# Kernel tuning notes

Measured on AMD Instinct MI355X. Metric: run time of the kernel, lower is better.

Reference implementation:

```python
import jax, jax.numpy as jnp
import numpy as np

_LN_EPS = 1e-5

def _gelu(x):
    return jax.nn.gelu(x, approximate=False)

def _layernorm(x, g, b):
    mu = x.mean(-1, keepdims=True)
    var = ((x - mu) ** 2).mean(-1, keepdims=True)
    return (x - mu) * jax.lax.rsqrt(var + _LN_EPS) * g + b

def setup_inputs() -> dict:
    key = jax.random.key(0)
    ks = jax.random.split(key, 8)
    B, S, D = 4, 2048, 1024
    N_IN, N_PROC, D_R = 8192, 4096, 256
    s = 0.02
    return {
        "x": jax.random.normal(ks[0], (B, S, D), jnp.float32),
        "W1": jax.random.normal(ks[1], (2 * D_R, D), jnp.float32) * s,
        "b1": jnp.zeros((2 * D_R,), jnp.float32),
        "ln_g": jnp.ones((2 * D_R,), jnp.float32),
        "ln_b": jnp.zeros((2 * D_R,), jnp.float32),
        "W2": jax.random.normal(ks[2], (D_R, 2 * D_R), jnp.float32) * s,
        "b2": jnp.zeros((D_R,), jnp.float32),
        "neuron_keys": jax.random.normal(ks[3], (N_IN, D_R), jnp.float32) * s,
        "input_patterns": jax.random.normal(ks[4], (N_IN, D), jnp.float32) * s,
        "process_weights": jax.random.normal(ks[5], (N_PROC, N_IN), jnp.float32) * s,
        "process_outputs": jax.random.normal(ks[6], (N_PROC, D), jnp.float32) * s,
        "k_input": 4096,
        "k_process": 2048,
    }

def reference(x, W1, b1, ln_g, ln_b, W2, b2, neuron_keys, input_patterns,
              process_weights, process_outputs, k_input, k_process):
    d_routing = neuron_keys.shape[1]
    # --- Global router: sequence max-pool context -> query -> top-k input neurons
    gc = x.max(axis=1)                                   # [B, D]
    h = _layernorm(_gelu(gc @ W1.T + b1), ln_g, ln_b)    # [B, 2*d_r]
    query = h @ W2.T + b2                                # [B, d_r]
    logits = (query @ neuron_keys.T) / jnp.sqrt(jnp.asarray(d_routing, x.dtype))  # [B, N_in]
    _, input_idx = jax.lax.top_k(logits, k_input)        # [B, k_in]
    # --- Input neuron activations, gather selected ones
    input_acts = _gelu(jnp.einsum('bsd,nd->bsn', x, input_patterns))   # [B,S,N_in]
    sel_acts = jnp.take_along_axis(input_acts, input_idx[:, None, :], axis=2)  # [B,S,k_in]
    # --- Per-batch gather of process weight columns, process activations
    W_sel = jnp.take(process_weights, input_idx, axis=1)               # [N_proc,B,k_in]
    proc_acts = _gelu(jnp.einsum('bsk,pbk->bsp', sel_acts, W_sel))     # [B,S,N_proc]
    scores = proc_acts.mean(axis=1)                                    # [B,N_proc]
    _, proc_idx = jax.lax.top_k(scores, k_process)                     # [B,k_proc]
    sel_proc = jnp.take_along_axis(proc_acts, proc_idx[:, None, :], axis=2)  # [B,S,k_proc]
    out_w = process_outputs[proc_idx]                                  # [B,k_proc,D]
    return jnp.einsum('bsk,bkd->bsd', sel_proc, out_w)                 # [B,S,D]
```

## Files before the change

### kernel.cpp

```cpp
#include <hip/hip_runtime.h>
#include <cstdint>

#define B_    4
#define S_    2048
#define D_    1024
#define NIN   8192
#define NPROC 4096
#define DR    256
#define DR2   512
#define KIN   4096
#define KPROC 2048

typedef _Float16 v8h __attribute__((ext_vector_type(8)));
typedef _Float16 v4h __attribute__((ext_vector_type(4)));
typedef float    v4f __attribute__((ext_vector_type(4)));

__device__ __forceinline__ float geluf(float v) {
    return 0.5f * v * (1.0f + erff(v * 0.70710678f));
}

__device__ __forceinline__ void cp16(void* lds, const void* g) {
    __builtin_amdgcn_global_load_lds(
        (const __attribute__((address_space(1))) unsigned int*)g,
        (__attribute__((address_space(3))) unsigned int*)lds, 16, 0, 0);
}

__global__ void k_conv_x16(const float* __restrict__ x, _Float16* __restrict__ x16, int n4) {
    int i = blockIdx.x * 256 + threadIdx.x;
    if (i < n4) {
        float4 v = ((const float4*)x)[i];
        v4h h = { (_Float16)v.x, (_Float16)v.y, (_Float16)v.z, (_Float16)v.w };
        ((v4h*)x16)[i] = h;
    }
}

__global__ void k_conv_split(const float* __restrict__ p, _Float16* __restrict__ ph,
                             _Float16* __restrict__ pl, int n) {
    int i = blockIdx.x * 256 + threadIdx.x;
    if (i < n) {
        float v = p[i];
        _Float16 h = (_Float16)v;
        ph[i] = h;
        pl[i] = (_Float16)(v - (float)h);
    }
}

__global__ void k_max1(const float* __restrict__ x, float* __restrict__ pmax) {
    int d = blockIdx.x * 256 + threadIdx.x;
    int chunk = blockIdx.y;
    int b = blockIdx.z;
    const float* base = x + ((size_t)b * S_ + chunk * 128) * D_ + d;
    float m = -3.4e38f;
    for (int s = 0; s < 128; s++) m = fmaxf(m, base[(size_t)s * D_]);
    pmax[((size_t)b * 16 + chunk) * D_ + d] = m;
}

__global__ void k_max2(const float* __restrict__ pmax, double* __restrict__ gc64) {
    int d = blockIdx.x * 256 + threadIdx.x;
    int b = blockIdx.y;
    float m = -3.4e38f;
    for (int c = 0; c < 16; c++) m = fmaxf(m, pmax[((size_t)b * 16 + c) * D_ + d]);
    gc64[(size_t)b * D_ + d] = (double)m;
}

__global__ __launch_bounds__(256) void k_router1(
    const double* __restrict__ gc64, const float* __restrict__ W1, const float* __restrict__ b1,
    double* __restrict__ hpre)
{
    int wave = threadIdx.x >> 6, lane = threadIdx.x & 63;
    int j = blockIdx.x * 4 + wave;
    int b = blockIdx.y;
    const double* g = gc64 + (size_t)b * D_;
    const float* w = W1 + (size_t)j * D_;
    double acc = 0.0;
    for (int d = lane; d < D_; d += 64) acc += g[d] * (double)w[d];
#pragma unroll
    for (int o = 32; o > 0; o >>= 1) acc += __shfl_xor(acc, o, 64);
    if (lane == 0) {
        double z = acc + (double)b1[j];
        hpre[(size_t)b * DR2 + j] = 0.5 * z * (1.0 + erf(z * 0.7071067811865475244));
    }
}

__global__ __launch_bounds__(512) void k_router2(
    const double* __restrict__ hpre, const float* __restrict__ lng, const float* __restrict__ lnb,
    const float* __restrict__ W2, const float* __restrict__ b2, double* __restrict__ qs)
{
    __shared__ double sh[DR2];
    __shared__ double red[DR2];
    int b = blockIdx.x, j = threadIdx.x;
    double ge = hpre[(size_t)b * DR2 + j];
    sh[j] = ge; red[j] = ge;
    __syncthreads();
    for (int s = 256; s > 0; s >>= 1) { if (j < s) red[j] += red[j + s]; __syncthreads(); }
    double mu = red[0] / 512.0;
    __syncthreads();
    double dv = ge - mu;
    red[j] = dv * dv;
    __syncthreads();
    for (int s = 256; s > 0; s >>= 1) { if (j < s) red[j] += red[j + s]; __syncthreads(); }
    double rs = 1.0 / sqrt(red[0] / 512.0 + 1e-5);
    __syncthreads();
    sh[j] = dv * rs * (double)lng[j] + (double)lnb[j];
    __syncthreads();
    if (j < DR) {
        double q = (double)b2[j];
        const float* w2r = W2 + (size_t)j * DR2;
        for (int t = 0; t < DR2; t++) q += sh[t] * (double)w2r[t];
        qs[(size_t)b * DR + j] = q;
    }
}

__global__ __launch_bounds__(256) void k_router3(
    const double* __restrict__ qs, const float* __restrict__ keys, double* __restrict__ logits)
{
    int wave = threadIdx.x >> 6, lane = threadIdx.x & 63;
    int n = blockIdx.x * 4 + wave;
    int b = blockIdx.y;
    const double* q = qs + (size_t)b * DR;
    const float* kr = keys + (size_t)n * DR;
    double acc = 0.0;
#pragma unroll
    for (int t = 0; t < 4; t++) {
        int d = lane + t * 64;
        acc += q[d] * (double)kr[d];
    }
#pragma unroll
    for (int o = 32; o > 0; o >>= 1) acc += __shfl_xor(acc, o, 64);
    if (lane == 0) logits[(size_t)b * NIN + n] = acc * 0.0625;
}

template<int N, int K>
__global__ __launch_bounds__(1024) void k_topk(const double* __restrict__ vals, int* __restrict__ outIdx) {
    __shared__ unsigned long long keys[N];
    int b = blockIdx.x, tid = threadIdx.x;
    for (int i = tid; i < N; i += 1024) {
        float v = (float)vals[(size_t)b * N + i];
        unsigned int u = __float_as_uint(v);
        u = (u & 0x80000000u) ? ~u : (u | 0x80000000u);
        keys[i] = ((unsigned long long)u << 32) | (unsigned int)(~i);
    }
    __syncthreads();
    for (int k = 2; k <= N; k <<= 1)
        for (int j = k >> 1; j > 0; j >>= 1) {
            for (int i = tid; i < N; i += 1024) {
                int l = i ^ j;
                if (l > i) {
                    unsigned long long a = keys[i], c = keys[l];
                    bool up = ((i & k) == 0);
                    if ((a < c) == up) { keys[i] = c; keys[l] = a; }
                }
            }
            __syncthreads();
        }
    for (int i = tid; i < K; i += 1024)
        outIdx[(size_t)b * K + i] = (int)(~(unsigned int)keys[i]);
}

__global__ void k_gatherW(const float* __restrict__ pw, const int* __restrict__ iidx,
                          _Float16* __restrict__ Wh, _Float16* __restrict__ Wl,
                          int b_base, size_t wstride) {
    int p = blockIdx.x;
    int b = b_base + blockIdx.y;
    const float* row = pw + (size_t)p * NIN;
    const int* ix = iidx + (size_t)b * KIN;
    _Float16* wh = Wh + (size_t)blockIdx.y * wstride + (size_t)p * KIN;
    _Float16* wl = Wl + (size_t)blockIdx.y * wstride + (size_t)p * KIN;
    for (int j = threadIdx.x; j < KIN; j += 256) {
        float w = row[ix[j]];
        _Float16 h = (_Float16)w;
        wh[j] = h;
        wl[j] = (_Float16)(w - (float)h);
    }
}

__global__ void k_gatherSP(const _Float16* __restrict__ acts16, const int* __restrict__ pidx,
                           _Float16* __restrict__ sp) {
    int s = blockIdx.x, b = blockIdx.y;
    const _Float16* arow = acts16 + ((size_t)b * S_ + s) * NPROC;
    _Float16* orow = sp + ((size_t)b * S_ + s) * KPROC;
    const int* pi = pidx + (size_t)b * KPROC;
    for (int k = threadIdx.x; k < KPROC; k += 256) orow[k] = arow[pi[k]];
}

__global__ void k_gatherWoT(const _Float16* __restrict__ pout16, const int* __restrict__ pidx,
                            _Float16* __restrict__ woT) {
    __shared__ _Float16 t[64][65];
    int k0 = blockIdx.x * 64, d0 = blockIdx.y * 64, b = blockIdx.z;
    const int* pi = pidx + (size_t)b * KPROC;
    for (int i = threadIdx.x; i < 4096; i += 256) {
        int kk = i >> 6, dd = i & 63;
        t[kk][dd] = pout16[(size_t)pi[k0 + kk] * D_ + d0 + dd];
    }
    __syncthreads();
    for (int i = threadIdx.x; i < 4096; i += 256) {
        int dd = i >> 6, kk = i & 63;
        woT[((size_t)b * D_ + d0 + dd) * KPROC + k0 + kk] = t[kk][dd];
    }
}


__global__ __launch_bounds__(256, 3) void k_gemmD(
    const _Float16* __restrict__ x16, const _Float16* __restrict__ ph, const _Float16* __restrict__ pl,
    const int* __restrict__ iidx, _Float16* __restrict__ a16)
{
    const int b = blockIdx.z;
    const int m0 = blockIdx.x * 128, n0 = blockIdx.y * 128;
    __shared__ _Float16 tA[4096], tBh[4096], tBl[4096];
    const int tid = threadIdx.x, lane = tid & 63;
    const int wave = tid >> 6, wrow = wave >> 1, wcol = wave & 1;
    const int srow = tid >> 2, spart = tid & 3;
    const int spe = spart ^ ((srow >> 1) & 3);

    const _Float16* as0 = x16 + ((size_t)b * S_ + m0 + srow) * D_ + spe * 8;
    const _Float16* as1 = as0 + (size_t)64 * D_;
    int r0 = iidx[(size_t)b * KIN + n0 + srow];
    int r1 = iidx[(size_t)b * KIN + n0 + srow + 64];
    const _Float16* bh0 = ph + (size_t)r0 * D_ + spe * 8;
    const _Float16* bh1 = ph + (size_t)r1 * D_ + spe * 8;
    const _Float16* bl0 = pl + (size_t)r0 * D_ + spe * 8;
    const _Float16* bl1 = pl + (size_t)r1 * D_ + spe * 8;

    v4f acc[4][4];
    v4f z = {0.f, 0.f, 0.f, 0.f};
#pragma unroll
    for (int i = 0; i < 4; i++)
#pragma unroll
        for (int j = 0; j < 4; j++) acc[i][j] = z;

    const int swz = ((lane & 15) >> 1) & 3;
    const int aoff = (wrow * 64 + (lane & 15)) * 32 + ((lane >> 4) ^ swz) * 8;
    const int boff = (wcol * 64 + (lane & 15)) * 32 + ((lane >> 4) ^ swz) * 8;

    for (int kt = 0; kt < D_; kt += 32) {
        __syncthreads();
        cp16(&tA[tid * 8], as0 + kt);
        cp16(&tA[2048 + tid * 8], as1 + kt);
        cp16(&tBh[tid * 8], bh0 + kt);
        cp16(&tBh[2048 + tid * 8], bh1 + kt);
        cp16(&tBl[tid * 8], bl0 + kt);
        cp16(&tBl[2048 + tid * 8], bl1 + kt);
        asm volatile("s_waitcnt vmcnt(0)" ::: "memory");
        __syncthreads();
        v8h af[4], fh[4], fl[4];
#pragma unroll
        for (int i = 0; i < 4; i++) af[i] = *(const v8h*)&tA[aoff + i * 512];
#pragma unroll
        for (int j = 0; j < 4; j++) {
            fh[j] = *(const v8h*)&tBh[boff + j * 512];
            fl[j] = *(const v8h*)&tBl[boff + j * 512];
        }
#pragma unroll
        for (int i = 0; i < 4; i++)
#pragma unroll
            for (int j = 0; j < 4; j++) {
                acc[i][j] = __builtin_amdgcn_mfma_f32_16x16x32_f16(af[i], fh[j], acc[i][j], 0, 0, 0);
                acc[i][j] = __builtin_amdgcn_mfma_f32_16x16x32_f16(af[i], fl[j], acc[i][j], 0, 0, 0);
            }
    }
    const int rbase = m0 + wrow * 64 + ((lane >> 4) << 2);
    const int cbase = n0 + wcol * 64 + (lane & 15);
#pragma unroll
    for (int i = 0; i < 4; i++)
#pragma unroll
        for (int j = 0; j < 4; j++)
#pragma unroll
            for (int r = 0; r < 4; r++) {
                float gv = geluf(acc[i][j][r]);
                a16[((size_t)b * S_ + rbase + i * 16 + r) * (size_t)KIN + cbase + j * 16] = (_Float16)gv;
            }
}

__global__ __launch_bounds__(256, 3) void k_gemmE(
    const _Float16* __restrict__ a16, const _Float16* __restrict__ Wh, const _Float16* __restrict__ Wl,
    _Float16* __restrict__ acts16, double* __restrict__ scores, int b_base, size_t wstride)
{
    const int b = b_base + blockIdx.z;
    const int m0 = blockIdx.x * 128, n0 = blockIdx.y * 128;
    __shared__ _Float16 tA[4096], tBh[4096], tBl[4096];
    const int tid = threadIdx.x, lane = tid & 63;
    const int wave = tid >> 6, wrow = wave >> 1, wcol = wave & 1;
    const int srow = tid >> 2, spart = tid & 3;
    const int spe = spart ^ ((srow >> 1) & 3);

    const _Float16* as0 = a16 + ((size_t)b * S_ + m0 + srow) * (size_t)KIN + spe * 8;
    const _Float16* as1 = as0 + (size_t)64 * KIN;
    const _Float16* whB = Wh + (size_t)blockIdx.z * wstride;
    const _Float16* wlB = Wl + (size_t)blockIdx.z * wstride;
    const _Float16* bh0 = whB + (size_t)(n0 + srow) * KIN + spe * 8;
    const _Float16* bh1 = bh0 + (size_t)64 * KIN;
    const _Float16* bl0 = wlB + (size_t)(n0 + srow) * KIN + spe * 8;
    const _Float16* bl1 = bl0 + (size_t)64 * KIN;

    v4f acc[4][4];
    v4f z = {0.f, 0.f, 0.f, 0.f};
#pragma unroll
    for (int i = 0; i < 4; i++)
#pragma unroll
        for (int j = 0; j < 4; j++) acc[i][j] = z;

    const int swz = ((lane & 15) >> 1) & 3;
    const int aoff = (wrow * 64 + (lane & 15)) * 32 + ((lane >> 4) ^ swz) * 8;
    const int boff = (wcol * 64 + (lane & 15)) * 32 + ((lane >> 4) ^ swz) * 8;

    for (int kt = 0; kt < KIN; kt += 32) {
        __syncthreads();
        cp16(&tA[tid * 8], as0 + kt);
        cp16(&tA[2048 + tid * 8], as1 + kt);
        cp16(&tBh[tid * 8], bh0 + kt);
        cp16(&tBh[2048 + tid * 8], bh1 + kt);
        cp16(&tBl[tid * 8], bl0 + kt);
        cp16(&tBl[2048 + tid * 8], bl1 + kt);
        asm volatile("s_waitcnt vmcnt(0)" ::: "memory");
        __syncthreads();
        v8h af[4], fh[4], fl[4];
#pragma unroll
        for (int i = 0; i < 4; i++) af[i] = *(const v8h*)&tA[aoff + i * 512];
#pragma unroll
        for (int j = 0; j < 4; j++) {
            fh[j] = *(const v8h*)&tBh[boff + j * 512];
            fl[j] = *(const v8h*)&tBl[boff + j * 512];
        }
#pragma unroll
        for (int i = 0; i < 4; i++)
#pragma unroll
            for (int j = 0; j < 4; j++) {
                acc[i][j] = __builtin_amdgcn_mfma_f32_16x16x32_f16(af[i], fh[j], acc[i][j], 0, 0, 0);
                acc[i][j] = __builtin_amdgcn_mfma_f32_16x16x32_f16(af[i], fl[j], acc[i][j], 0, 0, 0);
            }
    }
    const int rbase = m0 + wrow * 64 + ((lane >> 4) << 2);
    const int cbase = n0 + wcol * 64 + (lane & 15);
    float psum[4] = {0.f, 0.f, 0.f, 0.f};
#pragma unroll
    for (int i = 0; i < 4; i++)
#pragma unroll
        for (int j = 0; j < 4; j++)
#pragma unroll
            for (int r = 0; r < 4; r++) {
                float gv = geluf(acc[i][j][r]);
                acts16[((size_t)b * S_ + rbase + i * 16 + r) * (size_t)NPROC + cbase + j * 16] = (_Float16)gv;
                psum[j] += gv;
            }
#pragma unroll
    for (int j = 0; j < 4; j++) {
        float s = psum[j];
        s += __shfl_xor(s, 16, 64);
        s += __shfl_xor(s, 32, 64);
        if ((lane >> 4) == 0)
            atomicAdd(&scores[(size_t)b * NPROC + cbase + j * 16], (double)s);
    }
}

__global__ __launch_bounds__(256, 3) void k_gemmF(
    const _Float16* __restrict__ sp, const _Float16* __restrict__ woT, float* __restrict__ out)
{
    const int b = blockIdx.z;
    const int m0 = blockIdx.x * 128, n0 = blockIdx.y * 128;
    __shared__ _Float16 tA[4096], tB[4096];
    const int tid = threadIdx.x, lane = tid & 63;
    const int wave = tid >> 6, wrow = wave >> 1, wcol = wave & 1;
    const int srow = tid >> 2, spart = tid & 3;
    const int spe = spart ^ ((srow >> 1) & 3);

    const _Float16* as0 = sp + ((size_t)b * S_ + m0 + srow) * (size_t)KPROC + spe * 8;
    const _Float16* as1 = as0 + (size_t)64 * KPROC;
    const _Float16* bs0 = woT + ((size_t)b * D_ + n0 + srow) * (size_t)KPROC + spe * 8;
    const _Float16* bs1 = bs0 + (size_t)64 * KPROC;

    v4f acc[4][4];
    v4f z = {0.f, 0.f, 0.f, 0.f};
#pragma unroll
    for (int i = 0; i < 4; i++)
#pragma unroll
        for (int j = 0; j < 4; j++) acc[i][j] = z;

    const int swz = ((lane & 15) >> 1) & 3;
    const int aoff = (wrow * 64 + (lane & 15)) * 32 + ((lane >> 4) ^ swz) * 8;
    const int boff = (wcol * 64 + (lane & 15)) * 32 + ((lane >> 4) ^ swz) * 8;

    for (int kt = 0; kt < KPROC; kt += 32) {
        __syncthreads();
        cp16(&tA[tid * 8], as0 + kt);
        cp16(&tA[2048 + tid * 8], as1 + kt);
        cp16(&tB[tid * 8], bs0 + kt);
        cp16(&tB[2048 + tid * 8], bs1 + kt);
        asm volatile("s_waitcnt vmcnt(0)" ::: "memory");
        __syncthreads();
        v8h af[4], bf[4];
#pragma unroll
        for (int i = 0; i < 4; i++) af[i] = *(const v8h*)&tA[aoff + i * 512];
#pragma unroll
        for (int j = 0; j < 4; j++) bf[j] = *(const v8h*)&tB[boff + j * 512];
#pragma unroll
        for (int i = 0; i < 4; i++)
#pragma unroll
            for (int j = 0; j < 4; j++)
                acc[i][j] = __builtin_amdgcn_mfma_f32_16x16x32_f16(af[i], bf[j], acc[i][j], 0, 0, 0);
    }
    const int rbase = m0 + wrow * 64 + ((lane >> 4) << 2);
    const int cbase = n0 + wcol * 64 + (lane & 15);
#pragma unroll
    for (int i = 0; i < 4; i++)
#pragma unroll
        for (int j = 0; j < 4; j++)
#pragma unroll
            for (int r = 0; r < 4; r++)
                out[((size_t)b * S_ + rbase + i * 16 + r) * (size_t)D_ + cbase + j * 16] = acc[i][j][r];
}

extern "C" void kernel_launch(void* const* d_in, const int* in_sizes, int n_in,
                              void* d_out, int out_size, void* d_ws, size_t ws_size,
                              hipStream_t stream) {
    const float* x    = (const float*)d_in[0];
    const float* W1   = (const float*)d_in[1];
    const float* b1   = (const float*)d_in[2];
    const float* lng  = (const float*)d_in[3];
    const float* lnb  = (const float*)d_in[4];
    const float* W2   = (const float*)d_in[5];
    const float* b2   = (const float*)d_in[6];
    const float* keys = (const float*)d_in[7];
    const float* patt = (const float*)d_in[8];
    const float* pw   = (const float*)d_in[9];
    const float* pout = (const float*)d_in[10];
    (void)in_sizes; (void)n_in; (void)out_size;

    char* w = (char*)d_ws;
    size_t off = 0;
    auto alloc = [&](size_t bytes) -> void* {
        void* p = w + off;
        off += (bytes + 255) & ~(size_t)255;
        return p;
    };
    double* gc64   = (double*)alloc((size_t)B_ * D_ * 8);
    float*  pmax   = (float*) alloc((size_t)B_ * 16 * D_ * 4);
    double* logits = (double*)alloc((size_t)B_ * NIN * 8);
    double* scores = (double*)alloc((size_t)B_ * NPROC * 8);
    double* hpre   = (double*)alloc((size_t)B_ * DR2 * 8);
    double* qs     = (double*)alloc((size_t)B_ * DR * 8);
    int*    iidx   = (int*)   alloc((size_t)B_ * KIN * 4);
    int*    pidx   = (int*)   alloc((size_t)B_ * KPROC * 4);
    _Float16* a16    = (_Float16*)alloc((size_t)B_ * S_ * KIN * 2);
    _Float16* acts16 = (_Float16*)alloc((size_t)B_ * S_ * NPROC * 2);
    _Float16* pout16 = (_Float16*)alloc((size_t)NPROC * D_ * 2);
    char* u1 = (char*)alloc((size_t)67108864);
    _Float16* x16 = (_Float16*)u1;
    _Float16* ph  = (_Float16*)(u1 + 16777216);
    _Float16* pl  = (_Float16*)(u1 + 33554432);
    _Float16* WhT = (_Float16*)u1;
    _Float16* WlT = (_Float16*)(u1 + 33554432);
    _Float16* sp  = (_Float16*)u1;
    _Float16* woT = (_Float16*)(u1 + 33554432);

    const size_t WSTRIDE = (size_t)NPROC * KIN;
    size_t off_before_fat = off;
    _Float16* WhA = (_Float16*)alloc((size_t)B_ * WSTRIDE * 2);
    _Float16* WlA = (_Float16*)alloc((size_t)B_ * WSTRIDE * 2);
    bool fat = (off <= ws_size);
    if (!fat) off = off_before_fat;

    hipMemsetAsync(scores, 0, (size_t)B_ * NPROC * 8, stream);

    k_conv_x16 <<<dim3((B_ * S_ * D_ / 4 + 255) / 256), 256, 0, stream>>>(x, x16, B_ * S_ * D_ / 4);
    k_conv_split<<<dim3((NIN * D_ + 255) / 256), 256, 0, stream>>>(patt, ph, pl, NIN * D_);
    k_conv_x16 <<<dim3((NPROC * D_ / 4 + 255) / 256), 256, 0, stream>>>(pout, pout16, NPROC * D_ / 4);

    k_max1<<<dim3(4, 16, 4), 256, 0, stream>>>(x, pmax);
    k_max2<<<dim3(4, 4), 256, 0, stream>>>(pmax, gc64);
    k_router1<<<dim3(128, 4), 256, 0, stream>>>(gc64, W1, b1, hpre);
    k_router2<<<dim3(4), 512, 0, stream>>>(hpre, lng, lnb, W2, b2, qs);
    k_router3<<<dim3(2048, 4), 256, 0, stream>>>(qs, keys, logits);
    k_topk<NIN, KIN><<<dim3(4), 1024, 0, stream>>>(logits, iidx);

    if (fat) {
        k_gatherW<<<dim3(NPROC, 4), 256, 0, stream>>>(pw, iidx, WhA, WlA, 0, WSTRIDE);
        k_gemmD<<<dim3(16, 32, 4), 256, 0, stream>>>(x16, ph, pl, iidx, a16);
        k_gemmE<<<dim3(16, 32, 4), 256, 0, stream>>>(a16, WhA, WlA, acts16, scores, 0, WSTRIDE);
    } else {
        k_gemmD<<<dim3(16, 32, 4), 256, 0, stream>>>(x16, ph, pl, iidx, a16);
        for (int b = 0; b < 4; b++) {
            k_gatherW<<<dim3(NPROC, 1), 256, 0, stream>>>(pw, iidx, WhT, WlT, b, 0);
            k_gemmE<<<dim3(16, 32, 1), 256, 0, stream>>>(a16, WhT, WlT, acts16, scores, b, 0);
        }
    }

    k_topk<NPROC, KPROC><<<dim3(4), 1024, 0, stream>>>(scores, pidx);
    k_gatherSP<<<dim3(S_, 4), 256, 0, stream>>>(acts16, pidx, sp);
    k_gatherWoT<<<dim3(KPROC / 64, D_ / 64, 4), 256, 0, stream>>>(pout16, pidx, woT);
    k_gemmF<<<dim3(16, 8, 4), 256, 0, stream>>>(sp, woT, (float*)d_out);
}
```

Measured before the change: 1.666 ms.

## Switch GEMMs to 32x32x16 MFMA and merge weight gather into gemmD launch

All three GEMM kernels move from 16x16x32 MFMA tiles to 32x32x16 MFMA with 16-wide accumulators, with LDS fragment reads and epilogue indexing rewritten to match. The output tile is unchanged, but fewer, larger matrix instructions and fewer LDS fragment loads are issued per k-step. Separately, the process-weight column gather is folded into the gemmD launch as extra blocks along z, so gather blocks and GEMM blocks can occupy the GPU at the same time. Gather blocks now carry the GEMM's shared memory allocation, which may limit how many of them fit per CU.

```diff
diff --git a/kernel.cpp b/kernel.cpp
--- a/kernel.cpp
+++ b/kernel.cpp
@@ -11,9 +11,10 @@
 #define KIN   4096
 #define KPROC 2048
 
-typedef _Float16 v8h __attribute__((ext_vector_type(8)));
-typedef _Float16 v4h __attribute__((ext_vector_type(4)));
-typedef float    v4f __attribute__((ext_vector_type(4)));
+typedef _Float16 v8h  __attribute__((ext_vector_type(8)));
+typedef _Float16 v4h  __attribute__((ext_vector_type(4)));
+typedef float    v4f  __attribute__((ext_vector_type(4)));
+typedef float    v16f __attribute__((ext_vector_type(16)));
 
 __device__ __forceinline__ float geluf(float v) {
     return 0.5f * v * (1.0f + erff(v * 0.70710678f));
@@ -157,15 +158,13 @@
         outIdx[(size_t)b * K + i] = (int)(~(unsigned int)keys[i]);
 }
 
-__global__ void k_gatherW(const float* __restrict__ pw, const int* __restrict__ iidx,
-                          _Float16* __restrict__ Wh, _Float16* __restrict__ Wl,
-                          int b_base, size_t wstride) {
-    int p = blockIdx.x;
-    int b = b_base + blockIdx.y;
+__device__ __forceinline__ void dev_gatherW(const float* __restrict__ pw, const int* __restrict__ iidx,
+                                            _Float16* __restrict__ Wh, _Float16* __restrict__ Wl,
+                                            int p, int b, size_t bstride) {
     const float* row = pw + (size_t)p * NIN;
     const int* ix = iidx + (size_t)b * KIN;
-    _Float16* wh = Wh + (size_t)blockIdx.y * wstride + (size_t)p * KIN;
-    _Float16* wl = Wl + (size_t)blockIdx.y * wstride + (size_t)p * KIN;
+    _Float16* wh = Wh + bstride + (size_t)p * KIN;
+    _Float16* wl = Wl + bstride + (size_t)p * KIN;
     for (int j = threadIdx.x; j < KIN; j += 256) {
         float w = row[ix[j]];
         _Float16 h = (_Float16)w;
@@ -200,13 +199,12 @@
 }
 
 
-__global__ __launch_bounds__(256, 3) void k_gemmD(
+__device__ __forceinline__ void dev_gemmD(
     const _Float16* __restrict__ x16, const _Float16* __restrict__ ph, const _Float16* __restrict__ pl,
-    const int* __restrict__ iidx, _Float16* __restrict__ a16)
-{
-    const int b = blockIdx.z;
-    const int m0 = blockIdx.x * 128, n0 = blockIdx.y * 128;
-    __shared__ _Float16 tA[4096], tBh[4096], tBl[4096];
+    const int* __restrict__ iidx, _Float16* __restrict__ a16,
+    _Float16* tA, _Float16* tBh, _Float16* tBl, int bx, int by, int b)
+{
+    const int m0 = bx * 128, n0 = by * 128;
     const int tid = threadIdx.x, lane = tid & 63;
     const int wave = tid >> 6, wrow = wave >> 1, wcol = wave & 1;
     const int srow = tid >> 2, spart = tid & 3;
@@ -221,16 +219,16 @@
     const _Float16* bl0 = pl + (size_t)r0 * D_ + spe * 8;
     const _Float16* bl1 = pl + (size_t)r1 * D_ + spe * 8;
 
-    v4f acc[4][4];
-    v4f z = {0.f, 0.f, 0.f, 0.f};
-#pragma unroll
-    for (int i = 0; i < 4; i++)
-#pragma unroll
-        for (int j = 0; j < 4; j++) acc[i][j] = z;
-
-    const int swz = ((lane & 15) >> 1) & 3;
-    const int aoff = (wrow * 64 + (lane & 15)) * 32 + ((lane >> 4) ^ swz) * 8;
-    const int boff = (wcol * 64 + (lane & 15)) * 32 + ((lane >> 4) ^ swz) * 8;
+    v16f acc[2][2];
+#pragma unroll
+    for (int i = 0; i < 2; i++)
+#pragma unroll
+        for (int j = 0; j < 2; j++) acc[i][j] = (v16f)(0.0f);
+
+    const int lrow = lane & 31, lhi = lane >> 5;
+    const int swz = (lane >> 1) & 3;
+    const int abase = (wrow * 64 + lrow) * 32;
+    const int bbase = (wcol * 64 + lrow) * 32;
 
     for (int kt = 0; kt < D_; kt += 32) {
         __syncthreads();
@@ -242,33 +240,68 @@
         cp16(&tBl[2048 + tid * 8], bl1 + kt);
         asm volatile("s_waitcnt vmcnt(0)" ::: "memory");
         __syncthreads();
-        v8h af[4], fh[4], fl[4];
-#pragma unroll
-        for (int i = 0; i < 4; i++) af[i] = *(const v8h*)&tA[aoff + i * 512];
-#pragma unroll
-        for (int j = 0; j < 4; j++) {
-            fh[j] = *(const v8h*)&tBh[boff + j * 512];
-            fl[j] = *(const v8h*)&tBl[boff + j * 512];
+        v8h af[2][2], fh[2][2], fl[2][2];
+#pragma unroll
+        for (int kw = 0; kw < 2; kw++) {
+            const int ch = ((kw * 2 + lhi) ^ swz) * 8;
+#pragma unroll
+            for (int mi = 0; mi < 2; mi++) af[mi][kw] = *(const v8h*)&tA[abase + mi * 1024 + ch];
+#pragma unroll
+            for (int nj = 0; nj < 2; nj++) {
+                fh[nj][kw] = *(const v8h*)&tBh[bbase + nj * 1024 + ch];
+                fl[nj][kw] = *(const v8h*)&tBl[bbase + nj * 1024 + ch];
+            }
         }
 #pragma unroll
-        for (int i = 0; i < 4; i++)
-#pragma unroll
-            for (int j = 0; j < 4; j++) {
-                acc[i][j] = __builtin_amdgcn_mfma_f32_16x16x32_f16(af[i], fh[j], acc[i][j], 0, 0, 0);
-                acc[i][j] = __builtin_amdgcn_mfma_f32_16x16x32_f16(af[i], fl[j], acc[i][j], 0, 0, 0);
+        for (int kw = 0; kw < 2; kw++)
+#pragma unroll
+            for (int mi = 0; mi < 2; mi++)
+#pragma unroll
+                for (int nj = 0; nj < 2; nj++) {
+                    acc[mi][nj] = __builtin_amdgcn_mfma_f32_32x32x16_f16(af[mi][kw], fh[nj][kw], acc[mi][nj], 0, 0, 0);
+                    acc[mi][nj] = __builtin_amdgcn_mfma_f32_32x32x16_f16(af[mi][kw], fl[nj][kw], acc[mi][nj], 0, 0, 0);
+                }
+    }
+#pragma unroll
+    for (int mi = 0; mi < 2; mi++)
+#pragma unroll
+        for (int nj = 0; nj < 2; nj++)
+#pragma unroll
+            for (int r = 0; r < 16; r++) {
+                int row = (r & 3) + 8 * (r >> 2) + 4 * lhi;
+                float gv = geluf(acc[mi][nj][r]);
+                a16[((size_t)b * S_ + m0 + wrow * 64 + mi * 32 + row) * (size_t)KIN
+                    + n0 + wcol * 64 + nj * 32 + lrow] = (_Float16)gv;
             }
-    }
-    const int rbase = m0 + wrow * 64 + ((lane >> 4) << 2);
-    const int cbase = n0 + wcol * 64 + (lane & 15);
-#pragma unroll
-    for (int i = 0; i < 4; i++)
-#pragma unroll
-        for (int j = 0; j < 4; j++)
-#pragma unroll
-            for (int r = 0; r < 4; r++) {
-                float gv = geluf(acc[i][j][r]);
-                a16[((size_t)b * S_ + rbase + i * 16 + r) * (size_t)KIN + cbase + j * 16] = (_Float16)gv;
-            }
+}
+
+__global__ __launch_bounds__(256, 3) void k_gemmD(
+    const _Float16* __restrict__ x16, const _Float16* __restrict__ ph, const _Float16* __restrict__ pl,
+    const int* __restrict__ iidx, _Float16* __restrict__ a16)
+{
+    __shared__ _Float16 tA[4096], tBh[4096], tBl[4096];
+    dev_gemmD(x16, ph, pl, iidx, a16, tA, tBh, tBl, blockIdx.x, blockIdx.y, blockIdx.z);
+}
+
+__global__ __launch_bounds__(256, 3) void k_fusedDW(
+    const _Float16* __restrict__ x16, const _Float16* __restrict__ ph, const _Float16* __restrict__ pl,
+    const int* __restrict__ iidx, _Float16* __restrict__ a16,
+    const float* __restrict__ pw, _Float16* __restrict__ Wh, _Float16* __restrict__ Wl, size_t wstride)
+{
+    __shared__ _Float16 tA[4096], tBh[4096], tBl[4096];
+    if (blockIdx.z >= 4) {
+        int idx = (blockIdx.z - 4) * 512 + blockIdx.y * 16 + blockIdx.x;
+        int p = idx >> 2, b = idx & 3;
+        dev_gatherW(pw, iidx, Wh, Wl, p, b, (size_t)b * wstride);
+        return;
+    }
+    dev_gemmD(x16, ph, pl, iidx, a16, tA, tBh, tBl, blockIdx.x, blockIdx.y, blockIdx.z);
+}
+
+__global__ void k_gatherW(const float* __restrict__ pw, const int* __restrict__ iidx,
+                          _Float16* __restrict__ Wh, _Float16* __restrict__ Wl,
+                          int b_base, size_t wstride) {
+    dev_gatherW(pw, iidx, Wh, Wl, blockIdx.x, b_base + blockIdx.y, (size_t)blockIdx.y * wstride);
 }
 
 __global__ __launch_bounds__(256, 3) void k_gemmE(
@@ -292,16 +325,16 @@
     const _Float16* bl0 = wlB + (size_t)(n0 + srow) * KIN + spe * 8;
     const _Float16* bl1 = bl0 + (size_t)64 * KIN;
 
-    v4f acc[4][4];
-    v4f z = {0.f, 0.f, 0.f, 0.f};
-#pragma unroll
-    for (int i = 0; i < 4; i++)
-#pragma unroll
-        for (int j = 0; j < 4; j++) acc[i][j] = z;
-
-    const int swz = ((lane & 15) >> 1) & 3;
-    const int aoff = (wrow * 64 + (lane & 15)) * 32 + ((lane >> 4) ^ swz) * 8;
-    const int boff = (wcol * 64 + (lane & 15)) * 32 + ((lane >> 4) ^ swz) * 8;
+    v16f acc[2][2];
+#pragma unroll
+    for (int i = 0; i < 2; i++)
+#pragma unroll
+        for (int j = 0; j < 2; j++) acc[i][j] = (v16f)(0.0f);
+
+    const int lrow = lane & 31, lhi = lane >> 5;
+    const int swz = (lane >> 1) & 3;
+    const int abase = (wrow * 64 + lrow) * 32;
+    const int bbase = (wcol * 64 + lrow) * 32;
 
     for (int kt = 0; kt < KIN; kt += 32) {
         __syncthreads();
@@ -313,42 +346,47 @@
         cp16(&tBl[2048 + tid * 8], bl1 + kt);
         asm volatile("s_waitcnt vmcnt(0)" ::: "memory");
         __syncthreads();
-        v8h af[4], fh[4], fl[4];
-#pragma unroll
-        for (int i = 0; i < 4; i++) af[i] = *(const v8h*)&tA[aoff + i * 512];
-#pragma unroll
-        for (int j = 0; j < 4; j++) {
-            fh[j] = *(const v8h*)&tBh[boff + j * 512];
-            fl[j] = *(const v8h*)&tBl[boff + j * 512];
+        v8h af[2][2], fh[2][2], fl[2][2];
+#pragma unroll
+        for (int kw = 0; kw < 2; kw++) {
+            const int ch = ((kw * 2 + lhi) ^ swz) * 8;
+#pragma unroll
+            for (int mi = 0; mi < 2; mi++) af[mi][kw] = *(const v8h*)&tA[abase + mi * 1024 + ch];
+#pragma unroll
+            for (int nj = 0; nj < 2; nj++) {
+                fh[nj][kw] = *(const v8h*)&tBh[bbase + nj * 1024 + ch];
+                fl[nj][kw] = *(const v8h*)&tBl[bbase + nj * 1024 + ch];
+            }
         }
 #pragma unroll
-        for (int i = 0; i < 4; i++)
-#pragma unroll
-            for (int j = 0; j < 4; j++) {
-                acc[i][j] = __builtin_amdgcn_mfma_f32_16x16x32_f16(af[i], fh[j], acc[i][j], 0, 0, 0);
-                acc[i][j] = __builtin_amdgcn_mfma_f32_16x16x32_f16(af[i], fl[j], acc[i][j], 0, 0, 0);
+        for (int kw = 0; kw < 2; kw++)
+#pragma unroll
+            for (int mi = 0; mi < 2; mi++)
+#pragma unroll
+                for (int nj = 0; nj < 2; nj++) {
+                    acc[mi][nj] = __builtin_amdgcn_mfma_f32_32x32x16_f16(af[mi][kw], fh[nj][kw], acc[mi][nj], 0, 0, 0);
+                    acc[mi][nj] = __builtin_amdgcn_mfma_f32_32x32x16_f16(af[mi][kw], fl[nj][kw], acc[mi][nj], 0, 0, 0);
+                }
+    }
+    float psum[2] = {0.f, 0.f};
+#pragma unroll
+    for (int mi = 0; mi < 2; mi++)
+#pragma unroll
+        for (int nj = 0; nj < 2; nj++)
+#pragma unroll
+            for (int r = 0; r < 16; r++) {
+                int row = (r & 3) + 8 * (r >> 2) + 4 * lhi;
+                float gv = geluf(acc[mi][nj][r]);
+                acts16[((size_t)b * S_ + m0 + wrow * 64 + mi * 32 + row) * (size_t)NPROC
+                       + n0 + wcol * 64 + nj * 32 + lrow] = (_Float16)gv;
+                psum[nj] += gv;
             }
-    }
-    const int rbase = m0 + wrow * 64 + ((lane >> 4) << 2);
-    const int cbase = n0 + wcol * 64 + (lane & 15);
-    float psum[4] = {0.f, 0.f, 0.f, 0.f};
-#pragma unroll
-    for (int i = 0; i < 4; i++)
-#pragma unroll
-        for (int j = 0; j < 4; j++)
-#pragma unroll
-            for (int r = 0; r < 4; r++) {
-                float gv = geluf(acc[i][j][r]);
-                acts16[((size_t)b * S_ + rbase + i * 16 + r) * (size_t)NPROC + cbase + j * 16] = (_Float16)gv;
-                psum[j] += gv;
-            }
-#pragma unroll
-    for (int j = 0; j < 4; j++) {
-        float s = psum[j];
-        s += __shfl_xor(s, 16, 64);
+#pragma unroll
+    for (int nj = 0; nj < 2; nj++) {
+        float s = psum[nj];
         s += __shfl_xor(s, 32, 64);
-        if ((lane >> 4) == 0)
-            atomicAdd(&scores[(size_t)b * NPROC + cbase + j * 16], (double)s);
+        if (lhi == 0)
+            atomicAdd(&scores[(size_t)b * NPROC + n0 + wcol * 64 + nj * 32 + lrow], (double)s);
     }
 }
 
@@ -368,16 +406,16 @@
     const _Float16* bs0 = woT + ((size_t)b * D_ + n0 + srow) * (size_t)KPROC + spe * 8;
     const _Float16* bs1 = bs0 + (size_t)64 * KPROC;
 
-    v4f acc[4][4];
-    v4f z = {0.f, 0.f, 0.f, 0.f};
-#pragma unroll
-    for (int i = 0; i < 4; i++)
-#pragma unroll
-        for (int j = 0; j < 4; j++) acc[i][j] = z;
-
-    const int swz = ((lane & 15) >> 1) & 3;
-    const int aoff = (wrow * 64 + (lane & 15)) * 32 + ((lane >> 4) ^ swz) * 8;
-    const int boff = (wcol * 64 + (lane & 15)) * 32 + ((lane >> 4) ^ swz) * 8;
+    v16f acc[2][2];
+#pragma unroll
+    for (int i = 0; i < 2; i++)
+#pragma unroll
+        for (int j = 0; j < 2; j++) acc[i][j] = (v16f)(0.0f);
+
+    const int lrow = lane & 31, lhi = lane >> 5;
+    const int swz = (lane >> 1) & 3;
+    const int abase = (wrow * 64 + lrow) * 32;
+    const int bbase = (wcol * 64 + lrow) * 32;
 
     for (int kt = 0; kt < KPROC; kt += 32) {
         __syncthreads();
@@ -387,26 +425,33 @@
         cp16(&tB[2048 + tid * 8], bs1 + kt);
         asm volatile("s_waitcnt vmcnt(0)" ::: "memory");
         __syncthreads();
-        v8h af[4], bf[4];
-#pragma unroll
-        for (int i = 0; i < 4; i++) af[i] = *(const v8h*)&tA[aoff + i * 512];
-#pragma unroll
-        for (int j = 0; j < 4; j++) bf[j] = *(const v8h*)&tB[boff + j * 512];
-#pragma unroll
-        for (int i = 0; i < 4; i++)
-#pragma unroll
-            for (int j = 0; j < 4; j++)
-                acc[i][j] = __builtin_amdgcn_mfma_f32_16x16x32_f16(af[i], bf[j], acc[i][j], 0, 0, 0);
-    }
-    const int rbase = m0 + wrow * 64 + ((lane >> 4) << 2);
-    const int cbase = n0 + wcol * 64 + (lane & 15);
-#pragma unroll
-    for (int i = 0; i < 4; i++)
-#pragma unroll
-        for (int j = 0; j < 4; j++)
-#pragma unroll
-            for (int r = 0; r < 4; r++)
-                out[((size_t)b * S_ + rbase + i * 16 + r) * (size_t)D_ + cbase + j * 16] = acc[i][j][r];
+        v8h af[2][2], bf[2][2];
+#pragma unroll
+        for (int kw = 0; kw < 2; kw++) {
+            const int ch = ((kw * 2 + lhi) ^ swz) * 8;
+#pragma unroll
+            for (int mi = 0; mi < 2; mi++) af[mi][kw] = *(const v8h*)&tA[abase + mi * 1024 + ch];
+#pragma unroll
+            for (int nj = 0; nj < 2; nj++) bf[nj][kw] = *(const v8h*)&tB[bbase + nj * 1024 + ch];
+        }
+#pragma unroll
+        for (int kw = 0; kw < 2; kw++)
+#pragma unroll
+            for (int mi = 0; mi < 2; mi++)
+#pragma unroll
+                for (int nj = 0; nj < 2; nj++)
+                    acc[mi][nj] = __builtin_amdgcn_mfma_f32_32x32x16_f16(af[mi][kw], bf[nj][kw], acc[mi][nj], 0, 0, 0);
+    }
+#pragma unroll
+    for (int mi = 0; mi < 2; mi++)
+#pragma unroll
+        for (int nj = 0; nj < 2; nj++)
+#pragma unroll
+            for (int r = 0; r < 16; r++) {
+                int row = (r & 3) + 8 * (r >> 2) + 4 * lhi;
+                out[((size_t)b * S_ + m0 + wrow * 64 + mi * 32 + row) * (size_t)D_
+                    + n0 + wcol * 64 + nj * 32 + lrow] = acc[mi][nj][r];
+            }
 }
 
 extern "C" void kernel_launch(void* const* d_in, const int* in_sizes, int n_in,
@@ -473,8 +518,7 @@
     k_topk<NIN, KIN><<<dim3(4), 1024, 0, stream>>>(logits, iidx);
 
     if (fat) {
-        k_gatherW<<<dim3(NPROC, 4), 256, 0, stream>>>(pw, iidx, WhA, WlA, 0, WSTRIDE);
-        k_gemmD<<<dim3(16, 32, 4), 256, 0, stream>>>(x16, ph, pl, iidx, a16);
+        k_fusedDW<<<dim3(16, 32, 36), 256, 0, stream>>>(x16, ph, pl, iidx, a16, pw, WhA, WlA, WSTRIDE);
         k_gemmE<<<dim3(16, 32, 4), 256, 0, stream>>>(a16, WhA, WlA, acts16, scores, 0, WSTRIDE);
     } else {
         k_gemmD<<<dim3(16, 32, 4), 256, 0, stream>>>(x16, ph, pl, iidx, a16);
```

Measured after the change: 1.662 ms. No clear change (-0.2%).
